# Performance work log

Hardware: AMD Instinct MI355X
Metric: run time of the kernel (lower is better)

Reference implementation:

```python
import jax, jax.numpy as jnp
import numpy as np

B, T_ENC, D_IN = 8, 512, 512
T_DEC, ODIM = 150, 80
D_RNN, PRE, ATTN, LOC, K = 1024, 256, 128, 32, 31
ZONEOUT = 0.1


def setup_inputs() -> dict:
    key = jax.random.key(0)
    ks = jax.random.split(key, 24)
    s = 0.02
    n = jax.random.normal
    inp = {
        "memory": n(ks[0], (B, T_ENC, D_IN), jnp.float32),
        "memory_length": jax.random.randint(ks[1], (B,), 256, T_ENC + 1, jnp.int32),
        "targets": n(ks[2], (B, T_DEC, ODIM), jnp.float32),
        # location-sensitive attention params
        "W_mem": n(ks[3], (ATTN, D_IN), jnp.float32) * s,
        "W_q": n(ks[4], (ATTN, D_RNN), jnp.float32) * s,
        "W_loc": n(ks[5], (ATTN, LOC), jnp.float32) * s,
        "loc_filters": n(ks[6], (LOC, 1, K), jnp.float32) * s,
        "attn_v": n(ks[7], (ATTN,), jnp.float32) * s,
        "attn_b": jnp.zeros((ATTN,), jnp.float32),
        # prenet (80 -> 256 -> 256)
        "pre_W1": n(ks[8], (PRE, ODIM), jnp.float32) * s,
        "pre_b1": jnp.zeros((PRE,), jnp.float32),
        "pre_W2": n(ks[9], (PRE, PRE), jnp.float32) * s,
        "pre_b2": jnp.zeros((PRE,), jnp.float32),
        # LSTM layer 0: input = D_IN + PRE
        "Wi0": n(ks[10], (4 * D_RNN, D_IN + PRE), jnp.float32) * s,
        "Wh0": n(ks[11], (4 * D_RNN, D_RNN), jnp.float32) * s,
        "bl0": jnp.zeros((4 * D_RNN,), jnp.float32),
        # LSTM layer 1
        "Wi1": n(ks[12], (4 * D_RNN, D_RNN), jnp.float32) * s,
        "Wh1": n(ks[13], (4 * D_RNN, D_RNN), jnp.float32) * s,
        "bl1": jnp.zeros((4 * D_RNN,), jnp.float32),
        # projections from zcs = [h_last, att_c] of width D_RNN + D_IN
        "feat_W": n(ks[14], (ODIM, D_RNN + D_IN), jnp.float32) * s,
        "stop_W": n(ks[15], (1, D_RNN + D_IN), jnp.float32) * s,
        "stop_b": jnp.zeros((1,), jnp.float32),
    }
    return inp


def _lstm_cell(x, h, c, Wi, Wh, b):
    g = x @ Wi.T + h @ Wh.T + b
    i, f, gc, o = jnp.split(g, 4, axis=-1)  # torch LSTMCell gate order
    c_new = jax.nn.sigmoid(f) * c + jax.nn.sigmoid(i) * jnp.tanh(gc)
    h_new = jax.nn.sigmoid(o) * jnp.tanh(c_new)
    # zoneout (expected value / eval form)
    return (1.0 - ZONEOUT) * h_new + ZONEOUT * h, (1.0 - ZONEOUT) * c_new + ZONEOUT * c


def reference(memory, memory_length, targets, W_mem, W_q, W_loc, loc_filters,
              attn_v, attn_b, pre_W1, pre_b1, pre_W2, pre_b2,
              Wi0, Wh0, bl0, Wi1, Wh1, bl1, feat_W, stop_W, stop_b):
    b, t_enc, _ = memory.shape
    proc_mem = jnp.einsum('btd,ad->bta', memory, W_mem)           # [B,T,ATTN]
    mask = jnp.arange(t_enc)[None, :] < memory_length[:, None]    # [B,T]

    def step(carry, prev_out):
        h0, c0, h1, c1, att_cum = carry
        # location features: conv over cumulative attention weights
        f = jax.lax.conv_general_dilated(att_cum[:, None, :], loc_filters,
                                         (1,), 'SAME')            # [B,LOC,T]
        loc = jnp.einsum('bct,ac->bta', f, W_loc)                  # [B,T,ATTN]
        q = (h0 @ W_q.T)[:, None, :]                               # [B,1,ATTN]
        e = jnp.einsum('a,bta->bt', attn_v,
                       jnp.tanh(proc_mem + loc + q + attn_b))      # [B,T]
        att_w = jax.nn.softmax(jnp.where(mask, e, -1e9), axis=-1)
        att_c = jnp.einsum('bt,btd->bd', att_w, memory)            # [B,D_IN]
        # prenet on previous output (dropout off: deterministic reference)
        p = jax.nn.relu(prev_out @ pre_W1.T + pre_b1)
        p = jax.nn.relu(p @ pre_W2.T + pre_b2)
        x = jnp.concatenate([att_c, p], axis=1)                    # [B,D_IN+PRE]
        h0, c0 = _lstm_cell(x, h0, c0, Wi0, Wh0, bl0)
        h1, c1 = _lstm_cell(h0, h1, c1, Wi1, Wh1, bl1)
        zcs = jnp.concatenate([h1, att_c], axis=1)                 # use_concate=True
        out = zcs @ feat_W.T                                       # [B,ODIM]
        stop = zcs @ stop_W.T + stop_b                             # [B,1]
        return (h0, c0, h1, c1, att_cum + att_w), (out, stop, att_w)

    z = jnp.zeros((b, D_RNN), memory.dtype)
    init = (z, z, z, z, jnp.zeros((b, t_enc), memory.dtype))
    # teacher forcing: prev_out at step t is targets[t-1], zeros at t=0
    prev_outs = jnp.concatenate(
        [jnp.zeros((b, 1, ODIM), targets.dtype), targets[:, :-1]], axis=1)
    _, (outs, stops, att_ws) = jax.lax.scan(step, init,
                                            jnp.swapaxes(prev_outs, 0, 1))
    before_outs = jnp.swapaxes(outs, 0, 1)         # [B,T_dec,ODIM]
    stops = jnp.swapaxes(stops, 0, 1)[..., 0]      # [B,T_dec]
    att_ws = jnp.swapaxes(att_ws, 0, 1)            # [B,T_dec,T_enc]
    return before_outs, stops, att_ws
```

## Files before the change

kernel.cpp:

```cpp
#include <hip/hip_runtime.h>
#include <hip/hip_fp16.h>
#include <cstdint>
#include <cstddef>


#define NB 256
#define NT 512

#define Bz   8
#define TE   512
#define DINz 512
#define TDz  150
#define ODz  80
#define DRz  1024
#define PREz 256
#define ATz  128
#define LOCz 32
#define KFz  31

#define OF_P    0
#define OF_PM   307200
#define OF_Q    831488
#define OF_U    832512
#define OF_CUM  836608
#define OF_ATTC 840704
#define OF_S    848896
#define OF_INVS 848912
#define OF_H0   848928
#define OF_C0   857120
#define OF_H1   865312
#define OF_C1   873504
#define OF_GH0  881696
#define OF_GH1  914464
#define OF_BAR  947232

#define OFF_X0   0
#define OFF_X1   2048
#define OFF_EX   4096
#define OFF_EXG  4352
#define OFF_CW   4608
#define OFF_QS   4736
#define OFF_PART 4864
#define OFF_UU   5376
#define OFF_F    5632
#define OFF_V    9600
#define OFF_WA   9728
#define OFF_WB   22016
#define OFF_WG1  4608
#define OFF_WG2  20992
#define SM_TOTF  38400

#define AG __HIP_MEMORY_SCOPE_AGENT

__device__ __forceinline__ float ldg_sc1(const float* p){
  return __hip_atomic_load(p, __ATOMIC_RELAXED, AG);
}
__device__ __forceinline__ void stg_sc1(float* p, float v){
  __hip_atomic_store(p, v, __ATOMIC_RELAXED, AG);
}
__device__ __forceinline__ float4 ldg4_sc1(const float* p){
  float4 r; r.x=ldg_sc1(p); r.y=ldg_sc1(p+1); r.z=ldg_sc1(p+2); r.w=ldg_sc1(p+3);
  return r;
}
__device__ __forceinline__ float fsig_(float x){ return 1.f/(1.f + __expf(-x)); }
__device__ __forceinline__ float ftanh_(float x){
  x = fminf(10.f, fmaxf(-10.f, x));
  float e = __expf(2.f*x);
  return (e - 1.f) / (e + 1.f);
}

__device__ __forceinline__ void grid_barrier(int* bar, int target){
  asm volatile("s_waitcnt vmcnt(0) lgkmcnt(0)" ::: "memory");
  __syncthreads();
  const int tid = threadIdx.x;
  if (tid == 0)
    __hip_atomic_store(bar + (blockIdx.x << 4), target, __ATOMIC_RELAXED, AG);
  if (blockIdx.x == 255){
    for (;;){
      int ok = 1;
      if (tid < 256)
        ok = (__hip_atomic_load(bar + (tid << 4), __ATOMIC_RELAXED, AG) >= target);
      if (__syncthreads_and(ok)) break;
    }
    if (tid < 16)
      __hip_atomic_store(bar + 4096 + (tid << 4), target, __ATOMIC_RELAXED, AG);
  }
  if (tid == 0){
    int* ep = bar + 4096 + ((blockIdx.x >> 4) << 4);
    while (__hip_atomic_load(ep, __ATOMIC_RELAXED, AG) < target)
      __builtin_amdgcn_s_sleep(1);
  }
  __syncthreads();
}
__device__ __forceinline__ void grid_barrier_heavy(int* bar, int target){
  asm volatile("s_waitcnt vmcnt(0) lgkmcnt(0)" ::: "memory");
  __syncthreads();
  const int tid = threadIdx.x;
  if (tid == 0)
    __builtin_amdgcn_fence(__ATOMIC_RELEASE, "agent");
  __syncthreads();
  if (tid == 0)
    __hip_atomic_store(bar + (blockIdx.x << 4), target, __ATOMIC_RELAXED, AG);
  if (blockIdx.x == 255){
    for (;;){
      int ok = 1;
      if (tid < 256)
        ok = (__hip_atomic_load(bar + (tid << 4), __ATOMIC_RELAXED, AG) >= target);
      if (__syncthreads_and(ok)) break;
    }
    if (tid < 16)
      __hip_atomic_store(bar + 4096 + (tid << 4), target, __ATOMIC_RELAXED, AG);
  }
  if (tid == 0){
    int* ep = bar + 4096 + ((blockIdx.x >> 4) << 4);
    while (__hip_atomic_load(ep, __ATOMIC_RELAXED, AG) < target)
      __builtin_amdgcn_s_sleep(1);
    __builtin_amdgcn_fence(__ATOMIC_ACQUIRE, "agent");
  }
  __syncthreads();
}

template<int K, bool GM>
__device__ void load_wtile(float* dstf, const float* __restrict__ W, int base){
  __half* dst = (__half*)dstf;
  constexpr int KV = K >> 2;
  constexpr int NV = 32 * KV;
  for (int idx = threadIdx.x; idx < NV; idx += NT){
    int r = idx / KV;
    int c = (idx - r*KV) << 2;
    int grow = GM ? (((r>>3)<<10) + base + (r&7)) : (base + r);
    float4 w = *(const float4*)(W + (size_t)grow*K + c);
    __half* d = dst + (size_t)r*K + c;
    d[0] = __float2half_rn(w.x);
    d[1] = __float2half_rn(w.y);
    d[2] = __float2half_rn(w.z);
    d[3] = __float2half_rn(w.w);
  }
}

__device__ __forceinline__ float reduce_dot(float* sm, float (&acc)[2][8]){
  const int tid = threadIdx.x;
  const int s = tid & 31, pos = tid >> 5;
  #pragma unroll
  for (int i=0;i<2;++i){
    #pragma unroll
    for (int b=0;b<8;++b){
      float v = acc[i][b];
      v += __shfl_xor(v, 16, 64);
      v += __shfl_xor(v,  8, 64);
      v += __shfl_xor(v,  4, 64);
      v += __shfl_xor(v,  2, 64);
      v += __shfl_xor(v,  1, 64);
      acc[i][b] = v;
    }
  }
  if (s == 0){
    #pragma unroll
    for (int i=0;i<2;++i)
      #pragma unroll
      for (int b=0;b<8;++b)
        sm[OFF_EX + ((((pos<<1)+i)<<3) | b)] = acc[i][b];
  }
  __syncthreads();
  return (tid < 256) ? sm[OFF_EX + tid] : 0.f;
}

template<int K, int XMODE>
__device__ float gemm32x8_lds(float* sm, const __half* __restrict__ wlds,
                              const float* __restrict__ xsrc,
                              const float* __restrict__ attc_cur,
                              const float* __restrict__ S_cur,
                              const float* __restrict__ Pt)
{
  constexpr int NCH = K >> 8;
  const int tid = threadIdx.x;
  const int s = tid & 31, pos = tid >> 5;
  float acc[2][8];
  #pragma unroll
  for (int i=0;i<2;++i)
    #pragma unroll
    for (int b=0;b<8;++b) acc[i][b] = 0.f;

  const int xb = tid >> 6, xcol = (tid & 63) << 2;
  float4 xreg[NCH];
  if constexpr (XMODE == 0){
    #pragma unroll
    for (int ch=0; ch<NCH; ++ch)
      xreg[ch] = ldg4_sc1(xsrc + (size_t)xb*K + (ch<<8) + xcol);
  } else {
    float xsc = 1.f / ldg_sc1(S_cur + xb);
    #pragma unroll
    for (int ch=0; ch<2; ++ch){
      float4 v = ldg4_sc1(attc_cur + (xb<<9) + (ch<<8) + xcol);
      v.x*=xsc; v.y*=xsc; v.z*=xsc; v.w*=xsc;
      xreg[ch] = v;
    }
    xreg[2] = *(const float4*)(Pt + (xb<<8) + xcol);
  }
  *(float4*)&sm[OFF_X0 + (xb<<8) + xcol] = xreg[0];
  __syncthreads();
  #pragma unroll
  for (int ch=0; ch<NCH; ++ch){
    if (ch+1 < NCH)
      *(float4*)&sm[(((ch+1)&1) ? OFF_X1 : OFF_X0) + (xb<<8) + xcol] = xreg[(ch+1 < NCH) ? ch+1 : 0];
    const float* xbase = &sm[((ch&1) ? OFF_X1 : OFF_X0)];
    const __half* wch = wlds + (ch<<8);
    #pragma unroll
    for (int j=0;j<2;++j){
      const int k = (j<<7) + (s<<2);
      float4 xv[8];
      #pragma unroll
      for (int b=0;b<8;++b) xv[b] = *(const float4*)&xbase[(b<<8) + k];
      #pragma unroll
      for (int i=0;i<2;++i){
        const int row = (pos<<1) + i;
        uint2 w2 = *(const uint2*)&wch[(size_t)row*K + k];
        __half2 ha = *reinterpret_cast<const __half2*>(&w2.x);
        __half2 hb = *reinterpret_cast<const __half2*>(&w2.y);
        float2 fa = __half22float2(ha);
        float2 fb = __half22float2(hb);
        #pragma unroll
        for (int b=0;b<8;++b){
          acc[i][b] = fmaf(fa.x, xv[b].x, acc[i][b]);
          acc[i][b] = fmaf(fa.y, xv[b].y, acc[i][b]);
          acc[i][b] = fmaf(fb.x, xv[b].z, acc[i][b]);
          acc[i][b] = fmaf(fb.y, xv[b].w, acc[i][b]);
        }
      }
    }
    __syncthreads();
  }
  return reduce_dot(sm, acc);
}

__device__ float gemm32x8_gw(float* sm, const float* __restrict__ W, int rowbase,
                             const float* __restrict__ xsrc)
{
  const int tid = threadIdx.x;
  const int s = tid & 31, pos = tid >> 5;
  float acc[2][8];
  #pragma unroll
  for (int i=0;i<2;++i)
    #pragma unroll
    for (int b=0;b<8;++b) acc[i][b] = 0.f;
  const int xb = tid >> 6, xcol = (tid & 63) << 2;
  float4 xreg[4];
  #pragma unroll
  for (int ch=0; ch<4; ++ch)
    xreg[ch] = ldg4_sc1(xsrc + (size_t)xb*1024 + (ch<<8) + xcol);
  const float* w0 = W + (size_t)(rowbase + (pos<<1))*1024 + (s<<2);
  *(float4*)&sm[OFF_X0 + (xb<<8) + xcol] = xreg[0];
  __syncthreads();
  #pragma unroll
  for (int ch=0; ch<4; ++ch){
    float4 wr[2][2];
    #pragma unroll
    for (int j=0;j<2;++j)
      #pragma unroll
      for (int i=0;i<2;++i)
        wr[j][i] = *(const float4*)(w0 + (size_t)i*1024 + (ch<<8) + (j<<7));
    if (ch+1 < 4)
      *(float4*)&sm[(((ch+1)&1) ? OFF_X1 : OFF_X0) + (xb<<8) + xcol] = xreg[(ch+1<4)?ch+1:0];
    const float* xbase = &sm[((ch&1) ? OFF_X1 : OFF_X0)];
    #pragma unroll
    for (int j=0;j<2;++j){
      const int k = (j<<7) + (s<<2);
      float4 xv[8];
      #pragma unroll
      for (int b=0;b<8;++b) xv[b] = *(const float4*)&xbase[(b<<8) + k];
      #pragma unroll
      for (int i=0;i<2;++i){
        float4 wv = wr[j][i];
        #pragma unroll
        for (int b=0;b<8;++b){
          acc[i][b] = fmaf(wv.x, xv[b].x, acc[i][b]);
          acc[i][b] = fmaf(wv.y, xv[b].y, acc[i][b]);
          acc[i][b] = fmaf(wv.z, xv[b].z, acc[i][b]);
          acc[i][b] = fmaf(wv.w, xv[b].w, acc[i][b]);
        }
      }
    }
    __syncthreads();
  }
  return reduce_dot(sm, acc);
}

__device__ __forceinline__ float prefetch_gh(const float* gh, int u0){
  const int tid = threadIdx.x;
  if (tid >= 256) return 0.f;
  int row32 = tid >> 3, b = tid & 7;
  int gate = row32 >> 3, ul = row32 & 7;
  return ldg_sc1(&gh[(((gate<<10) + u0 + ul)<<3) + b]);
}
__device__ __forceinline__ float prefetch_h(const float* h, int u0){
  const int tid = threadIdx.x;
  if (tid >= 64) return 0.f;
  return ldg_sc1(&h[((tid&7)<<10) + u0 + (tid>>3)]);
}

__device__ void lstm_epilogue(float* sm, float dot, float ghb,
                              const float* __restrict__ bias, float hold,
                              float* __restrict__ h, float* __restrict__ c, int u0)
{
  const int tid = threadIdx.x;
  if (tid < 256){
    int row32 = tid >> 3;
    int gate = row32 >> 3, ul = row32 & 7;
    sm[OFF_EXG + tid] = dot + bias[(gate<<10) + u0 + ul] + ghb;
  }
  __syncthreads();
  if (tid < 64){
    float gi = sm[OFF_EXG + tid];
    float gf = sm[OFF_EXG + 64 + tid];
    float gg = sm[OFF_EXG + 128 + tid];
    float go = sm[OFF_EXG + 192 + tid];
    int ul2 = tid >> 3, b2 = tid & 7;
    int hi = (b2<<10) + u0 + ul2;
    float co = c[hi];
    float cn = fsig_(gf)*co + fsig_(gi)*ftanh_(gg);
    float hn = fsig_(go)*ftanh_(cn);
    c[hi] = 0.9f*cn + 0.1f*co;
    stg_sc1(&h[hi], 0.9f*hn + 0.1f*hold);
  }
}

__device__ void outstop_wave(int rr, int tp, int par,
    const float* __restrict__ feat_W, const float* __restrict__ stop_W,
    const float* __restrict__ stop_b, const float* __restrict__ h1,
    const float* __restrict__ attc, const float* __restrict__ iSw,
    float* __restrict__ d_out)
{
  if (rr >= 648) return;
  int b = rr / 81, r = rr - 81*b;
  int lane = threadIdx.x & 63;
  const float4* Wr = (const float4*)((r < 80) ? (feat_W + (size_t)r*1536) : stop_W);
  float inv = ldg_sc1(iSw + (par<<3) + b);
  float acc = 0.f, acc2 = 0.f;
  #pragma unroll
  for (int j=0;j<4;++j){
    int p = lane + (j<<6);
    float4 w = Wr[p], x = ldg4_sc1(h1 + (b<<10) + (p<<2));
    acc = fmaf(w.x,x.x, fmaf(w.y,x.y, fmaf(w.z,x.z, fmaf(w.w,x.w, acc))));
  }
  #pragma unroll
  for (int j=4;j<6;++j){
    int p = lane + (j<<6);
    float4 w = Wr[p], x = ldg4_sc1(attc + (par<<12) + (b<<9) + ((p-256)<<2));
    acc2 = fmaf(w.x,x.x, fmaf(w.y,x.y, fmaf(w.z,x.z, fmaf(w.w,x.w, acc2))));
  }
  acc += acc2 * inv;
  acc += __shfl_down(acc, 32, 64);
  acc += __shfl_down(acc, 16, 64);
  acc += __shfl_down(acc,  8, 64);
  acc += __shfl_down(acc,  4, 64);
  acc += __shfl_down(acc,  2, 64);
  acc += __shfl_down(acc,  1, 64);
  if (lane == 0){
    if (r < 80) d_out[((size_t)b*TDz + tp)*ODz + r] = acc;
    else        d_out[96000 + (size_t)b*TDz + tp] = acc + stop_b[0];
  }
}

extern "C" __global__ void __launch_bounds__(NT, 1) dec_kernel(
  const float* __restrict__ memory, const int* __restrict__ mlen, const float* __restrict__ targets,
  const float* __restrict__ W_mem, const float* __restrict__ W_q, const float* __restrict__ W_loc,
  const float* __restrict__ loc_f, const float* __restrict__ attn_v, const float* __restrict__ attn_b,
  const float* __restrict__ pre_W1, const float* __restrict__ pre_b1,
  const float* __restrict__ pre_W2, const float* __restrict__ pre_b2,
  const float* __restrict__ Wi0, const float* __restrict__ Wh0, const float* __restrict__ bl0,
  const float* __restrict__ Wi1, const float* __restrict__ Wh1, const float* __restrict__ bl1,
  const float* __restrict__ feat_W, const float* __restrict__ stop_W, const float* __restrict__ stop_b,
  float* __restrict__ d_out, float* __restrict__ ws)
{
  __shared__ float sm[SM_TOTF];
  const int blk = blockIdx.x, tid = threadIdx.x;

  float* Pw   = ws + OF_P;
  float* pmT  = ws + OF_PM;
  float* qw   = ws + OF_Q;
  float* uw   = ws + OF_U;
  float* cum  = ws + OF_CUM;
  float* attc = ws + OF_ATTC;
  float* Sw   = ws + OF_S;
  float* iSw  = ws + OF_INVS;
  float* h0 = ws + OF_H0; float* c0 = ws + OF_C0;
  float* h1 = ws + OF_H1; float* c1 = ws + OF_C1;
  float* gh0 = ws + OF_GH0; float* gh1 = ws + OF_GH1;
  int* bar = (int*)(ws + OF_BAR);
  int bt = 0;

  const bool is_attn = (blk < 64);
  const int ab  = blk >> 3;
  const int ai0 = (blk & 7) << 6;
  const int il  = tid & 63;
  const int ag  = tid >> 6;

  {
    const int gs = NB*NT;
    const int gid = blk*NT + tid;
    for (int i = gid; i < 98304; i += gs) h0[i] = 0.f;
    for (int i = gid; i < 1024;  i += gs) qw[i]  = 0.f;
    for (int i = gid; i < 4096;  i += gs) cum[i] = 0.f;
    for (int i = gid; i < 8192;  i += gs) attc[i] = 0.f;
    if (gid < 32) Sw[gid] = 0.f;

    if (blk < 124){
      load_wtile<768, true >(&sm[OFF_WA], Wi0, blk<<3);
      load_wtile<1024,false>(&sm[OFF_WB], Wh0, blk<<5);
    } else if (blk < 128){
      load_wtile<768, true >(&sm[OFF_WA], Wi0, blk<<3);
      load_wtile<1024,false>(&sm[OFF_WB], W_q, (blk-124)<<5);
    } else {
      load_wtile<1024,false>(&sm[OFF_WG1], Wh1, (blk-128)<<5);
      load_wtile<1024,true >(&sm[OFF_WG2], Wi1, (blk-128)<<3);
    }

    if (is_attn){
      float pacc[16];
      #pragma unroll
      for (int j=0;j<16;++j) pacc[j] = 0.f;
      for (int dc=0; dc<4; ++dc){
        for (int idx = tid; idx < 8192; idx += NT){
          int r = idx >> 7, d = idx & 127;
          sm[r*129 + d] = memory[(size_t)((ab<<9)+ai0+r)*DINz + (dc<<7) + d];
        }
        __syncthreads();
        #pragma unroll
        for (int j=0;j<16;++j){
          int a = (ag<<4) + j;
          const float* wr = W_mem + (size_t)a*DINz + (dc<<7);
          const float* mr = &sm[il*129];
          float acc = 0.f;
          for (int d=0; d<128; d+=4){
            acc = fmaf(mr[d  ], wr[d  ], acc);
            acc = fmaf(mr[d+1], wr[d+1], acc);
            acc = fmaf(mr[d+2], wr[d+2], acc);
            acc = fmaf(mr[d+3], wr[d+3], acc);
          }
          pacc[j] += acc;
        }
        __syncthreads();
      }
      #pragma unroll
      for (int j=0;j<16;++j){
        int a = (ag<<4) + j;
        pmT[((size_t)blk<<13) + (a<<6) + il] = pacc[j] + attn_b[a];
      }
      for (int idx = tid; idx < ATz*KFz; idx += NT){
        int a = idx / KFz, k = idx - a*KFz;
        float s2 = 0.f;
        #pragma unroll
        for (int c2=0;c2<LOCz;++c2) s2 = fmaf(W_loc[(a<<5)+c2], loc_f[c2*KFz+k], s2);
        sm[OFF_F + idx] = s2;
      }
      if (tid < 128) sm[OFF_V + tid] = attn_v[tid];
      __syncthreads();
    }

    const int th = tid >> 8, t2 = tid & 255, base = th << 9;
    for (int it=0; it<3; ++it){
      int pp = (blk<<1) + th + (it<<9);
      bool act = pp < 1200;
      if (act && t2 < ODz){
        int tt = pp >> 3, bb = pp & 7;
        sm[base + t2] = (tt==0) ? 0.f : targets[((size_t)bb*TDz + (tt-1))*ODz + t2];
      }
      __syncthreads();
      if (act){
        float a1 = pre_b1[t2];
        for (int k=0;k<ODz;++k) a1 = fmaf(pre_W1[t2*ODz+k], sm[base+k], a1);
        sm[base + 128 + t2] = fmaxf(a1, 0.f);
      }
      __syncthreads();
      if (act){
        float a2 = pre_b2[t2];
        for (int k=0;k<PREz;++k) a2 = fmaf(pre_W2[(t2<<8)+k], sm[base+128+k], a2);
        Pw[((size_t)pp<<8) + t2] = fmaxf(a2, 0.f);
      }
      __syncthreads();
    }
  }
  grid_barrier_heavy(bar, ++bt);

  for (int t = 0; t < TDz; ++t){
    const int cur = t & 1, prv = cur ^ 1;

    if (is_attn){
      if (tid < 94){
        int gi = ai0 - 15 + tid;
        sm[OFF_CW + tid] = (gi >= 0 && gi < TE) ? ldg_sc1(&cum[(ab<<9)+gi]) : 0.f;
      }
      if (tid < 128) sm[OFF_QS + tid] = ldg_sc1(&qw[(tid<<3) + ab]);
      __syncthreads();
      float part = 0.f;
      #pragma unroll
      for (int j=0;j<16;++j){
        int a = (ag<<4) + j;
        const float* fb = &sm[OFF_F + a*KFz];
        float conv = 0.f;
        #pragma unroll
        for (int k=0;k<KFz;++k) conv = fmaf(fb[k], sm[OFF_CW + il + k], conv);
        float pv = pmT[((size_t)blk<<13) + (a<<6) + il];
        part = fmaf(sm[OFF_V + a], ftanh_(pv + sm[OFF_QS + a] + conv), part);
      }
      sm[OFF_PART + (il<<3) + ag] = part;
      __syncthreads();
      if (tid < 64){
        float e = 0.f;
        #pragma unroll
        for (int k=0;k<8;++k) e += sm[OFF_PART + (tid<<3) + k];
        int gi = ai0 + tid;
        float uu = (gi < mlen[ab]) ? __expf(e) : 0.f;
        stg_sc1(&uw[(ab<<9)+gi], uu);
        sm[OFF_UU + tid] = uu;
      }
      __syncthreads();
      if (tid == 0){
        float ssum = 0.f;
        #pragma unroll
        for (int k=0;k<64;++k) ssum += sm[OFF_UU + k];
        atomicAdd(&Sw[(cur<<3)+ab], ssum);
      }
      {
        float acc = 0.f;
        const float* mrow = memory + (size_t)((ab<<9)+ai0)*DINz + tid;
        #pragma unroll 4
        for (int i=0;i<64;++i)
          acc = fmaf(sm[OFF_UU + i], mrow[(size_t)i*DINz], acc);
        atomicAdd(&attc[(cur<<12) + (ab<<9) + tid], acc);
      }
    } else if (blk < 68){
      const int tile = 124 + (blk - 64);
      float dot = gemm32x8_gw(sm, Wh0, tile<<5, h0);
      if (tid < 256) stg_sc1(&gh0[(tile<<8) + tid], dot);
    } else if (blk >= 128){
      const int tile = blk - 128;
      float dot = gemm32x8_lds<1024,0>(sm, (const __half*)&sm[OFF_WG1], h1,
                                       nullptr, nullptr, nullptr);
      if (tid < 256) stg_sc1(&gh1[(tile<<8) + tid], dot);
    }
    grid_barrier(bar, ++bt);

    if (blk < 128){
      const int u0 = blk << 3;
      float ghb  = prefetch_gh(gh0, u0);
      float hold = prefetch_h(h0, u0);
      float dot = gemm32x8_lds<768,1>(sm, (const __half*)&sm[OFF_WA], nullptr,
                                      attc + (cur<<12), Sw + (cur<<3),
                                      Pw + ((size_t)t<<11));
      lstm_epilogue(sm, dot, ghb, bl0, hold, h0, c0, u0);
    } else if (blk < 136){
      const int b = blk - 128;
      float Sv = __hip_atomic_load(&Sw[(cur<<3)+b], __ATOMIC_RELAXED, AG);
      float inv = 1.f / Sv;
      if (tid == 0) stg_sc1(&iSw[(cur<<3)+b], inv);
      for (int i = tid; i < TE; i += NT){
        float u = ldg_sc1(&uw[(b<<9)+i]);
        float w = u * inv;
        d_out[97200 + ((size_t)b*TDz + t)*TE + i] = w;
        stg_sc1(&cum[(b<<9)+i], ldg_sc1(&cum[(b<<9)+i]) + w);
      }
    } else if (blk < 217){
      if (t > 0)
        outstop_wave((blk-136)*8 + (tid>>6), t-1, prv,
                     feat_W, stop_W, stop_b, h1, attc, iSw, d_out);
    }
    grid_barrier(bar, ++bt);

    if (blk < 124){
      float dot = gemm32x8_lds<1024,0>(sm, (const __half*)&sm[OFF_WB], h0,
                                       nullptr, nullptr, nullptr);
      if (tid < 256) stg_sc1(&gh0[(blk<<8) + tid], dot);
    } else if (blk < 128){
      const int rt = blk - 124;
      float dot = gemm32x8_lds<1024,0>(sm, (const __half*)&sm[OFF_WB], h0,
                                       nullptr, nullptr, nullptr);
      if (tid < 256) stg_sc1(&qw[(rt<<8) + tid], dot);
      const int zbase = (prv<<12) + (rt<<10);
      for (int i = tid; i < 1024; i += NT) stg_sc1(&attc[zbase + i], 0.f);
      if (rt == 0 && tid < 8) stg_sc1(&Sw[(prv<<3)+tid], 0.f);
    } else {
      const int u0 = (blk - 128) << 3;
      float ghb  = prefetch_gh(gh1, u0);
      float hold = prefetch_h(h1, u0);
      float dot = gemm32x8_lds<1024,0>(sm, (const __half*)&sm[OFF_WG2], h0,
                                       nullptr, nullptr, nullptr);
      lstm_epilogue(sm, dot, ghb, bl1, hold, h1, c1, u0);
    }
    grid_barrier(bar, ++bt);
  }

  if (blk >= 136 && blk < 217)
    outstop_wave((blk-136)*8 + (tid>>6), TDz-1, 1,
                 feat_W, stop_W, stop_b, h1, attc, iSw, d_out);
}

extern "C" void kernel_launch(void* const* d_in, const int* in_sizes, int n_in,
                              void* d_out, int out_size, void* d_ws, size_t ws_size,
                              hipStream_t stream)
{
  (void)in_sizes; (void)n_in; (void)out_size; (void)ws_size;
  (void)hipMemsetAsync((char*)d_ws + (size_t)OF_BAR*4, 0, 18432, stream);
  dec_kernel<<<dim3(NB), dim3(NT), 0, stream>>>(
    (const float*)d_in[0],  (const int*)d_in[1],   (const float*)d_in[2],
    (const float*)d_in[3],  (const float*)d_in[4],  (const float*)d_in[5],
    (const float*)d_in[6],  (const float*)d_in[7],  (const float*)d_in[8],
    (const float*)d_in[9],  (const float*)d_in[10], (const float*)d_in[11], (const float*)d_in[12],
    (const float*)d_in[13], (const float*)d_in[14], (const float*)d_in[15],
    (const float*)d_in[16], (const float*)d_in[17], (const float*)d_in[18],
    (const float*)d_in[19], (const float*)d_in[20], (const float*)d_in[21],
    (float*)d_out, (float*)d_ws);
}
```

Measured before the change: 5.175 ms.

## Spread attention over 128 blocks and fold the Wh0 tail rows into the layer-1 phase

Attention scoring and context accumulation now run on 128 blocks, each covering 32 encoder positions instead of 64, which roughly halves per-block work in the first phase of every decoder step. The four blocks that used to compute the last 128 rows of the Wh0·h0 product with a separate global-memory GEMM are freed for attention. Those rows are now computed in the third phase by blocks 128–255, one row each, using a wave-shuffle reduction over the freshly written h0. The trade-off is twice as many attention atomics, plus extra global loads of fp32 weights in the layer-1 phase.

```diff
diff --git a/kernel.cpp b/kernel.cpp
--- a/kernel.cpp
+++ b/kernel.cpp
@@ -233,58 +233,6 @@
   return reduce_dot(sm, acc);
 }
 
-__device__ float gemm32x8_gw(float* sm, const float* __restrict__ W, int rowbase,
-                             const float* __restrict__ xsrc)
-{
-  const int tid = threadIdx.x;
-  const int s = tid & 31, pos = tid >> 5;
-  float acc[2][8];
-  #pragma unroll
-  for (int i=0;i<2;++i)
-    #pragma unroll
-    for (int b=0;b<8;++b) acc[i][b] = 0.f;
-  const int xb = tid >> 6, xcol = (tid & 63) << 2;
-  float4 xreg[4];
-  #pragma unroll
-  for (int ch=0; ch<4; ++ch)
-    xreg[ch] = ldg4_sc1(xsrc + (size_t)xb*1024 + (ch<<8) + xcol);
-  const float* w0 = W + (size_t)(rowbase + (pos<<1))*1024 + (s<<2);
-  *(float4*)&sm[OFF_X0 + (xb<<8) + xcol] = xreg[0];
-  __syncthreads();
-  #pragma unroll
-  for (int ch=0; ch<4; ++ch){
-    float4 wr[2][2];
-    #pragma unroll
-    for (int j=0;j<2;++j)
-      #pragma unroll
-      for (int i=0;i<2;++i)
-        wr[j][i] = *(const float4*)(w0 + (size_t)i*1024 + (ch<<8) + (j<<7));
-    if (ch+1 < 4)
-      *(float4*)&sm[(((ch+1)&1) ? OFF_X1 : OFF_X0) + (xb<<8) + xcol] = xreg[(ch+1<4)?ch+1:0];
-    const float* xbase = &sm[((ch&1) ? OFF_X1 : OFF_X0)];
-    #pragma unroll
-    for (int j=0;j<2;++j){
-      const int k = (j<<7) + (s<<2);
-      float4 xv[8];
-      #pragma unroll
-      for (int b=0;b<8;++b) xv[b] = *(const float4*)&xbase[(b<<8) + k];
-      #pragma unroll
-      for (int i=0;i<2;++i){
-        float4 wv = wr[j][i];
-        #pragma unroll
-        for (int b=0;b<8;++b){
-          acc[i][b] = fmaf(wv.x, xv[b].x, acc[i][b]);
-          acc[i][b] = fmaf(wv.y, xv[b].y, acc[i][b]);
-          acc[i][b] = fmaf(wv.z, xv[b].z, acc[i][b]);
-          acc[i][b] = fmaf(wv.w, xv[b].w, acc[i][b]);
-        }
-      }
-    }
-    __syncthreads();
-  }
-  return reduce_dot(sm, acc);
-}
-
 __device__ __forceinline__ float prefetch_gh(const float* gh, int u0){
   const int tid = threadIdx.x;
   if (tid >= 256) return 0.f;
@@ -389,11 +337,11 @@
   int* bar = (int*)(ws + OF_BAR);
   int bt = 0;
 
-  const bool is_attn = (blk < 64);
-  const int ab  = blk >> 3;
-  const int ai0 = (blk & 7) << 6;
-  const int il  = tid & 63;
-  const int ag  = tid >> 6;
+  const bool is_attn = (blk < 128);
+  const int ab  = blk >> 4;
+  const int ai0 = (blk & 15) << 5;
+  const int il  = tid & 31;
+  const int ag  = tid >> 5;
 
   {
     const int gs = NB*NT;
@@ -416,18 +364,18 @@
     }
 
     if (is_attn){
-      float pacc[16];
+      float pacc[8];
       #pragma unroll
-      for (int j=0;j<16;++j) pacc[j] = 0.f;
+      for (int j=0;j<8;++j) pacc[j] = 0.f;
       for (int dc=0; dc<4; ++dc){
-        for (int idx = tid; idx < 8192; idx += NT){
+        for (int idx = tid; idx < 4096; idx += NT){
           int r = idx >> 7, d = idx & 127;
           sm[r*129 + d] = memory[(size_t)((ab<<9)+ai0+r)*DINz + (dc<<7) + d];
         }
         __syncthreads();
         #pragma unroll
-        for (int j=0;j<16;++j){
-          int a = (ag<<4) + j;
+        for (int j=0;j<8;++j){
+          int a = (ag<<3) + j;
           const float* wr = W_mem + (size_t)a*DINz + (dc<<7);
           const float* mr = &sm[il*129];
           float acc = 0.f;
@@ -442,9 +390,9 @@
         __syncthreads();
       }
       #pragma unroll
-      for (int j=0;j<16;++j){
-        int a = (ag<<4) + j;
-        pmT[((size_t)blk<<13) + (a<<6) + il] = pacc[j] + attn_b[a];
+      for (int j=0;j<8;++j){
+        int a = (ag<<3) + j;
+        pmT[((size_t)blk<<12) + (a<<5) + il] = pacc[j] + attn_b[a];
       }
       for (int idx = tid; idx < ATz*KFz; idx += NT){
         int a = idx / KFz, k = idx - a*KFz;
@@ -486,7 +434,7 @@
     const int cur = t & 1, prv = cur ^ 1;
 
     if (is_attn){
-      if (tid < 94){
+      if (tid < 62){
         int gi = ai0 - 15 + tid;
         sm[OFF_CW + tid] = (gi >= 0 && gi < TE) ? ldg_sc1(&cum[(ab<<9)+gi]) : 0.f;
       }
@@ -494,21 +442,21 @@
       __syncthreads();
       float part = 0.f;
       #pragma unroll
-      for (int j=0;j<16;++j){
-        int a = (ag<<4) + j;
+      for (int j=0;j<8;++j){
+        int a = (ag<<3) + j;
         const float* fb = &sm[OFF_F + a*KFz];
         float conv = 0.f;
         #pragma unroll
         for (int k=0;k<KFz;++k) conv = fmaf(fb[k], sm[OFF_CW + il + k], conv);
-        float pv = pmT[((size_t)blk<<13) + (a<<6) + il];
+        float pv = pmT[((size_t)blk<<12) + (a<<5) + il];
         part = fmaf(sm[OFF_V + a], ftanh_(pv + sm[OFF_QS + a] + conv), part);
       }
-      sm[OFF_PART + (il<<3) + ag] = part;
-      __syncthreads();
-      if (tid < 64){
+      sm[OFF_PART + (il<<4) + ag] = part;
+      __syncthreads();
+      if (tid < 32){
         float e = 0.f;
         #pragma unroll
-        for (int k=0;k<8;++k) e += sm[OFF_PART + (tid<<3) + k];
+        for (int k=0;k<16;++k) e += sm[OFF_PART + (tid<<4) + k];
         int gi = ai0 + tid;
         float uu = (gi < mlen[ab]) ? __expf(e) : 0.f;
         stg_sc1(&uw[(ab<<9)+gi], uu);
@@ -518,22 +466,18 @@
       if (tid == 0){
         float ssum = 0.f;
         #pragma unroll
-        for (int k=0;k<64;++k) ssum += sm[OFF_UU + k];
+        for (int k=0;k<32;++k) ssum += sm[OFF_UU + k];
         atomicAdd(&Sw[(cur<<3)+ab], ssum);
       }
       {
         float acc = 0.f;
         const float* mrow = memory + (size_t)((ab<<9)+ai0)*DINz + tid;
-        #pragma unroll 4
-        for (int i=0;i<64;++i)
+        #pragma unroll 8
+        for (int i=0;i<32;++i)
           acc = fmaf(sm[OFF_UU + i], mrow[(size_t)i*DINz], acc);
         atomicAdd(&attc[(cur<<12) + (ab<<9) + tid], acc);
       }
-    } else if (blk < 68){
-      const int tile = 124 + (blk - 64);
-      float dot = gemm32x8_gw(sm, Wh0, tile<<5, h0);
-      if (tid < 256) stg_sc1(&gh0[(tile<<8) + tid], dot);
-    } else if (blk >= 128){
+    } else {
       const int tile = blk - 128;
       float dot = gemm32x8_lds<1024,0>(sm, (const __half*)&sm[OFF_WG1], h1,
                                        nullptr, nullptr, nullptr);
@@ -581,6 +525,25 @@
       if (rt == 0 && tid < 8) stg_sc1(&Sw[(prv<<3)+tid], 0.f);
     } else {
       const int u0 = (blk - 128) << 3;
+      const int blkL = blk - 128;
+      {
+        const int xb = tid >> 6, xcol = (tid & 63) << 2;
+        const float* wr = Wh0 + (size_t)(3968 + blkL)*1024;
+        float tp_ = 0.f;
+        #pragma unroll
+        for (int c=0;c<4;++c){
+          float4 w = *(const float4*)(wr + (c<<8) + xcol);
+          float4 x = ldg4_sc1(h0 + (xb<<10) + (c<<8) + xcol);
+          tp_ = fmaf(w.x,x.x, fmaf(w.y,x.y, fmaf(w.z,x.z, fmaf(w.w,x.w, tp_))));
+        }
+        tp_ += __shfl_down(tp_, 32, 64);
+        tp_ += __shfl_down(tp_, 16, 64);
+        tp_ += __shfl_down(tp_,  8, 64);
+        tp_ += __shfl_down(tp_,  4, 64);
+        tp_ += __shfl_down(tp_,  2, 64);
+        tp_ += __shfl_down(tp_,  1, 64);
+        if ((tid & 63) == 0) stg_sc1(&gh0[((3968 + blkL)<<3) + xb], tp_);
+      }
       float ghb  = prefetch_gh(gh1, u0);
       float hold = prefetch_h(h1, u0);
       float dot = gemm32x8_lds<1024,0>(sm, (const __half*)&sm[OFF_WG2], h0,
```

Measured after the change: 4.777 ms. -7.7%, faster.
